# Kernel optimization log

Hardware: AMD Instinct MI355X
Metric: run time of the kernel (lower is better)

The kernel has to match this reference:

```python
import jax, jax.numpy as jnp
import numpy as np

BIG_NUMBER = 1e7   # repo constant used to mask padded adjacency slots
MAX_ITERS = 32     # params['flow_iters']


def _build_graph(B, N, D, valid_deg, seed=0):
    """Random d-regular-ish graph: each valid slot d holds a permutation of nodes,
    so every node has exactly `valid_deg` in-edges. in_indices[b,v,d] = (b,u,s)
    such that adj[b,u,s] == v. Padded slots (d >= valid_deg) hold the sentinel N
    and their in_indices point to a padded (near-zero-weight) flow entry."""
    rng = np.random.default_rng(seed)
    adj = np.full((B, N, D), N, dtype=np.int32)
    in_idx = np.zeros((B, N, D, 3), dtype=np.int32)
    in_idx[..., 0] = np.arange(B, dtype=np.int32)[:, None, None]
    in_idx[..., 2] = valid_deg  # padded slots -> flow[b, 0, valid_deg] (weight ~ 0)
    for b in range(B):
        for d in range(valid_deg):
            perm = rng.permutation(N).astype(np.int32)
            adj[b, :, d] = perm                      # edge u -> perm[u] via slot d
            inv = np.argsort(perm).astype(np.int32)  # inv[v] = u with perm[u] == v
            in_idx[b, :, d, 1] = inv
            in_idx[b, :, d, 2] = d
    return jnp.asarray(adj), jnp.asarray(in_idx)


def setup_inputs():
    B, N, D, VALID = 4, 100000, 16, 12
    key = jax.random.key(0)
    k1, k2 = jax.random.split(key)
    adj_lst, in_indices = _build_graph(B, N, D, VALID)
    return {
        "flow_proportions": jax.random.normal(k1, (B, N, D), dtype=jnp.float32),
        "demands": jax.random.normal(k2, (B, N, 1), dtype=jnp.float32),
        "adj_lst": adj_lst,
        "in_indices": in_indices,
        "num_nodes": N,
    }


def reference(flow_proportions, demands, adj_lst, in_indices, num_nodes):
    # --- masked softmax over neighbor slots (padded slots get -BIG_NUMBER) ---
    mask = (adj_lst == num_nodes).astype(flow_proportions.dtype)   # [B,N,D]
    masked = flow_proportions - BIG_NUMBER * mask
    weights = jax.nn.softmax(masked, axis=-1)                      # normalized_weights

    # --- mcf_solver: iterate flow <- weights * relu(inflow - demand) ---
    bidx = in_indices[..., 0]   # [B,N,D] batch index
    src = in_indices[..., 1]    # [B,N,D] source node of d-th in-edge
    slot = in_indices[..., 2]   # [B,N,D] slot of this node in source's adj list

    def step(flow, _):
        # gather incoming edge flows, sum -> inflow per node [B,N,1]
        inflow = flow[bidx, src, slot].sum(axis=-1, keepdims=True)
        new_flow = weights * jax.nn.relu(inflow - demands)
        return new_flow, None

    flow, _ = jax.lax.scan(step, jnp.zeros_like(weights), None, length=MAX_ITERS)
    # flow_cost (loss) = sum over nodes/slots of cost_fn(flow) = flow**2 here:
    # flow_cost = jnp.sum(flow * flow, axis=(1, 2))
    return flow
```

## Files before the change

kernel.cpp:

```cpp
#include <hip/hip_runtime.h>

#define DEG 16
#define E12 12
#define MAX_ITERS 32
#define BLK 1024
#define NCH 5
#define LDSH 20000
#define JMAX 96

typedef float f32x4 __attribute__((ext_vector_type(4)));

__device__ __forceinline__ float ld_sc0(const float* p) {
    return __hip_atomic_load((float*)p, __ATOMIC_RELAXED, __HIP_MEMORY_SCOPE_AGENT);
}
__device__ __forceinline__ unsigned ld_u32_sc0(const unsigned* p) {
    return __hip_atomic_load((unsigned*)p, __ATOMIC_RELAXED, __HIP_MEMORY_SCOPE_AGENT);
}
__device__ __forceinline__ void st_u32_sc0(unsigned* p, unsigned v) {
    __hip_atomic_store(p, v, __ATOMIC_RELAXED, __HIP_MEMORY_SCOPE_AGENT);
}

__device__ __forceinline__ f32x4 ld4_nw(const f32x4* p) {
    f32x4 v;
    asm volatile("global_load_dwordx4 %0, %1, off sc0" : "=v"(v) : "v"(p));
    return v;
}
__device__ __forceinline__ float ld1_l2(const float* p) {
    float v;
    asm volatile("global_load_dword %0, %1, off sc0\n\ts_waitcnt vmcnt(0)"
                 : "=v"(v) : "v"(p) : "memory");
    return v;
}
__device__ __forceinline__ void wait_vm0() {
    asm volatile("s_waitcnt vmcnt(0)" ::: "memory");
    __builtin_amdgcn_sched_barrier(0);
}

__device__ __forceinline__ int get_xcd() {
    unsigned x;
    asm volatile("s_getreg_b32 %0, hwreg(HW_REG_XCC_ID)" : "=s"(x));
    return (int)(x & 7u);
}

__device__ __forceinline__ void grid_barrier(unsigned* cnt, unsigned* gen,
                                             unsigned target, unsigned nblocks) {
    __syncthreads();
    if (threadIdx.x == 0) {
        __threadfence();
        unsigned arrived = __hip_atomic_fetch_add(cnt, 1u, __ATOMIC_ACQ_REL,
                                                  __HIP_MEMORY_SCOPE_AGENT);
        if (arrived == nblocks - 1u) {
            __hip_atomic_store(cnt, 0u, __ATOMIC_RELAXED, __HIP_MEMORY_SCOPE_AGENT);
            __hip_atomic_fetch_add(gen, 1u, __ATOMIC_RELEASE, __HIP_MEMORY_SCOPE_AGENT);
        } else {
            while (__hip_atomic_load(gen, __ATOMIC_RELAXED,
                                     __HIP_MEMORY_SCOPE_AGENT) < target)
                __builtin_amdgcn_s_sleep(2);
        }
        __threadfence();
    }
    __syncthreads();
}

__device__ __forceinline__ void xcd_barrier(unsigned* cnt, unsigned* gen,
                                            unsigned target, unsigned nblocks) {
    __syncthreads();
    if (threadIdx.x == 0) {
        unsigned arrived = __hip_atomic_fetch_add(cnt, 1u, __ATOMIC_RELEASE,
                                                  __HIP_MEMORY_SCOPE_WORKGROUP);
        if (arrived == nblocks - 1u) {
            __hip_atomic_store(cnt, 0u, __ATOMIC_RELAXED,
                               __HIP_MEMORY_SCOPE_WORKGROUP);
            __hip_atomic_fetch_add(gen, 1u, __ATOMIC_RELEASE,
                                   __HIP_MEMORY_SCOPE_WORKGROUP);
        } else {
            while (ld_u32_sc0(gen) < target)
                __builtin_amdgcn_s_sleep(2);
        }
    }
    __syncthreads();
}

__device__ __forceinline__ void softmax_row(const float* __restrict__ fp,
                                            const int* __restrict__ adj,
                                            float* __restrict__ wout,
                                            size_t base, int N) {
    const float4* f4 = (const float4*)(fp + base);
    const int4*   a4 = (const int4*)(adj + base);
    float v[DEG];
#pragma unroll
    for (int k = 0; k < DEG / 4; ++k) {
        float4 f = f4[k];
        int4   a = a4[k];
        v[4*k+0] = (a.x == N) ? f.x - 1e7f : f.x;
        v[4*k+1] = (a.y == N) ? f.y - 1e7f : f.y;
        v[4*k+2] = (a.z == N) ? f.z - 1e7f : f.z;
        v[4*k+3] = (a.w == N) ? f.w - 1e7f : f.w;
    }
    float m = v[0];
#pragma unroll
    for (int j = 1; j < DEG; ++j) m = fmaxf(m, v[j]);
    float s = 0.f;
#pragma unroll
    for (int j = 0; j < DEG; ++j) { v[j] = __expf(v[j] - m); s += v[j]; }
    float inv = 1.f / s;
    float4* w4 = (float4*)(wout + base);
#pragma unroll
    for (int k = 0; k < DEG / 4; ++k) {
        float4 o;
        o.x = v[4*k+0] * inv;
        o.y = v[4*k+1] * inv;
        o.z = v[4*k+2] * inv;
        o.w = v[4*k+3] * inv;
        w4[k] = o;
    }
}

__device__ __forceinline__ float node_acc12(const int* __restrict__ es,
                                            const float* __restrict__ ew,
                                            const float* __restrict__ Rc) {
    const int4*   s4 = (const int4*)es;
    const float4* w4 = (const float4*)ew;
    int4 a = s4[0], b = s4[1], c = s4[2];
    float4 x = w4[0], y = w4[1], z = w4[2];
    float acc;
    acc  = x.x * Rc[a.x];  acc += x.y * Rc[a.y];
    acc += x.z * Rc[a.z];  acc += x.w * Rc[a.w];
    acc += y.x * Rc[b.x];  acc += y.y * Rc[b.y];
    acc += y.z * Rc[b.z];  acc += y.w * Rc[b.w];
    acc += z.x * Rc[c.x];  acc += z.y * Rc[c.y];
    acc += z.z * Rc[c.z];  acc += z.w * Rc[c.w];
    return acc;
}

__device__ __forceinline__ void scale_row(float* __restrict__ wout, int g, float r) {
    float4* w4 = (float4*)(wout + (size_t)g * DEG);
#pragma unroll
    for (int k = 0; k < DEG / 4; ++k) {
        float4 v = w4[k];
        v.x *= r; v.y *= r; v.z *= r; v.w *= r;
        w4[k] = v;
    }
}

__device__ __forceinline__ void stage_issue(const float* src, int ce, int tid,
                                            f32x4* pv) {
    const int n4 = ce >> 2;
    const f32x4* s4 = (const f32x4*)src;
#pragma unroll
    for (int k = 0; k < 5; ++k) {
        int i4 = tid + k * BLK;
        if (i4 < n4) pv[k] = ld4_nw(s4 + i4);
    }
}
__device__ __forceinline__ void stage_write(float* L, const float* src, int ce,
                                            int tid, const f32x4* pv) {
    const int n4 = ce >> 2;
    f32x4* l4 = (f32x4*)L;
#pragma unroll
    for (int k = 0; k < 5; ++k) {
        int i4 = tid + k * BLK;
        if (i4 < n4) l4[i4] = pv[k];
    }
    for (int i = (n4 << 2) + tid; i < ce; i += BLK)
        L[i] = ld1_l2(src + i);
}

__global__ __launch_bounds__(BLK, 4)
void fused10_k(const float* __restrict__ fp, const int* __restrict__ adj,
               const int* __restrict__ in_idx, const float* __restrict__ dem,
               const int* __restrict__ nn, float* __restrict__ wout,
               char* __restrict__ wsb, int nodes) {
    __shared__ __align__(16) float lds2[2][LDSH];
    __shared__ int s_xcd, s_rank, s_mode, s_part, s_jbad;
    __shared__ int s_cm[NCH];
    __shared__ int s_off[NCH + 1];

    unsigned* g_cnt  = (unsigned*)(wsb);
    unsigned* g_gen  = (unsigned*)(wsb + 128);
    unsigned* blkcnt = (unsigned*)(wsb + 2304);
    unsigned* ovf    = (unsigned*)(wsb + 2432);
    unsigned* jovf   = (unsigned*)(wsb + 2436);
    int*   e_src   = (int*)(wsb + 4096);
    float* e_w     = (float*)(wsb + 4096 + (size_t)nodes * E12 * 4);
    float* Rf0     = (float*)((char*)e_w + (size_t)nodes * E12 * 4);
    float* Rf1     = Rf0 + nodes;
    float* slices  = Rf1 + nodes;
    uint2* regions = (uint2*)((char*)(slices) + (size_t)nodes * 16);

    const int N   = *nn;
    const int tid = (int)threadIdx.x;
    const int T   = (int)gridDim.x * BLK;
    const unsigned nblocks = gridDim.x;
    unsigned gb = 0;

    if (tid == 0) {
        int x = get_xcd();
        s_xcd  = x;
        s_rank = (int)__hip_atomic_fetch_add(&blkcnt[x], 1u, __ATOMIC_RELAXED,
                                             __HIP_MEMORY_SCOPE_AGENT);
    }
    __syncthreads();
    const int my_xcd  = s_xcd;
    const int my_rank = s_rank;

#pragma unroll
    for (int rep = 0; rep < 2; ++rep) {
        int g = (int)blockIdx.x * BLK + tid + rep * T;
        if (g < nodes) softmax_row(fp, adj, wout, (size_t)g * DEG, N);
    }
    grid_barrier(g_cnt, g_gen, ++gb, nblocks);

#pragma unroll
    for (int rep = 0; rep < 2; ++rep) {
        int g = (int)blockIdx.x * BLK + tid + rep * T;
        if (g >= nodes) continue;
        const int gbat = g / N;
        const int4* t4 = (const int4*)(in_idx + (size_t)g * 48);
        int cb[16], cs[16], cl[16];
#pragma unroll
        for (int q = 0; q < 4; ++q) {
            int4 qa = t4[3*q + 0];
            int4 qb = t4[3*q + 1];
            int4 qc = t4[3*q + 2];
            cb[4*q+0] = qa.x; cs[4*q+0] = qa.y; cl[4*q+0] = qa.z;
            cb[4*q+1] = qa.w; cs[4*q+1] = qb.x; cl[4*q+1] = qb.y;
            cb[4*q+2] = qb.z; cs[4*q+2] = qb.w; cl[4*q+2] = qc.x;
            cb[4*q+3] = qc.y; cs[4*q+3] = qc.z; cl[4*q+3] = qc.w;
        }
        float cw[16];
#pragma unroll
        for (int k = 0; k < 16; ++k)
            cw[k] = wout[((size_t)cb[k] * N + cs[k]) * DEG + cl[k]];
        bool bad = (cw[12] != 0.f) || (cw[13] != 0.f) ||
                   (cw[14] != 0.f) || (cw[15] != 0.f);
#pragma unroll
        for (int k = 0; k < E12; ++k)
            bad = bad || (cb[k] != gbat) || ((unsigned)cs[k] >= (unsigned)N);
        if (bad) st_u32_sc0(ovf, 1u);
        int4*   es4 = (int4*)(e_src + (size_t)g * E12);
        float4* ew4 = (float4*)(e_w + (size_t)g * E12);
        es4[0] = make_int4(cs[0], cs[1], cs[2], cs[3]);
        es4[1] = make_int4(cs[4], cs[5], cs[6], cs[7]);
        es4[2] = make_int4(cs[8], cs[9], cs[10], cs[11]);
        ew4[0] = make_float4(cw[0], cw[1], cw[2], cw[3]);
        ew4[1] = make_float4(cw[4], cw[5], cw[6], cw[7]);
        ew4[2] = make_float4(cw[8], cw[9], cw[10], cw[11]);
    }
    grid_barrier(g_cnt, g_gen, ++gb, nblocks);

    const int npb   = (N + 31) >> 5;
    const int chunk = (((N + NCH - 1) / NCH) + 3) & ~3;
    if (tid == 0) {
        unsigned cc[8];
#pragma unroll
        for (int x = 0; x < 8; ++x) cc[x] = ld_u32_sc0(&blkcnt[x]);
        bool ok = (4 * N == nodes) && (N > 0) && (N % 4 == 0) &&
                  (npb <= 4 * BLK) && (chunk <= LDSH) &&
                  (ld_u32_sc0(ovf) == 0u);
#pragma unroll
        for (int p = 0; p < 4; ++p)
            ok = ok && (cc[2*p] >= 32u || cc[2*p+1] >= 32u);
        s_mode = ok ? 1 : 0;
        s_part = (ok && cc[my_xcd] >= 32u && my_rank < 32) ? 1 : 0;
    }
    __syncthreads();
    const bool fast = (s_mode == 1);
    const bool part = (s_part == 1);

    if (fast) {
        const int batch = my_xcd >> 1;
        const int lbase = my_rank * npb;
        const int lim   = min(lbase + npb, N);
        float d[4];
        int   lno[4];
        bool  act[4];
        float r[4];
        unsigned long long mycnt = 0;
        uint2* reg = regions + (size_t)(my_xcd * 32 + my_rank) * (JMAX * BLK);

        if (part) {
            if (tid < NCH) s_cm[tid] = 0;
            __syncthreads();
            const int b1 = chunk, b2 = 2 * chunk, b3 = 3 * chunk, b4 = 4 * chunk;
            int c0 = 0, c1 = 0, c2 = 0, c3 = 0, c4 = 0;
#pragma unroll
            for (int s = 0; s < 4; ++s) {
                int l = lbase + s * BLK + tid;
                lno[s] = l;
                act[s] = (l < lim);
                d[s] = 0.f;
                if (act[s]) {
                    int g = batch * N + l;
                    d[s] = dem[g];
                    const int* es = e_src + (size_t)g * E12;
#pragma unroll
                    for (int k = 0; k < E12; ++k) {
                        int src = es[k];
                        int c = (src >= b1) + (src >= b2) + (src >= b3) +
                                (src >= b4);
                        c0 += (c == 0); c1 += (c == 1); c2 += (c == 2);
                        c3 += (c == 3); c4 += (c == 4);
                    }
                }
            }
            atomicMax(&s_cm[0], c0); atomicMax(&s_cm[1], c1);
            atomicMax(&s_cm[2], c2); atomicMax(&s_cm[3], c3);
            atomicMax(&s_cm[4], c4);
            __syncthreads();
            if (tid == 0) {
                s_off[0] = 0;
#pragma unroll
                for (int c = 0; c < NCH; ++c) s_off[c + 1] = s_off[c] + s_cm[c];
                if (s_off[NCH] > JMAX) st_u32_sc0(jovf, 1u);
            }
            __syncthreads();
            if (s_off[NCH] <= JMAX) {
                int cur0 = s_off[0], cur1 = s_off[1], cur2 = s_off[2],
                    cur3 = s_off[3], cur4 = s_off[4];
#pragma unroll
                for (int s = 0; s < 4; ++s) {
                    if (!act[s]) continue;
                    int g = batch * N + lno[s];
                    const int*   es = e_src + (size_t)g * E12;
                    const float* ew = e_w + (size_t)g * E12;
#pragma unroll
                    for (int k = 0; k < E12; ++k) {
                        int src = es[k];
                        float w = ew[k];
                        int c = (src >= b1) + (src >= b2) + (src >= b3) +
                                (src >= b4);
                        int j = (c == 0) ? cur0 : (c == 1) ? cur1
                               : (c == 2) ? cur2 : (c == 3) ? cur3 : cur4;
                        reg[(size_t)j * BLK + tid] =
                            make_uint2((unsigned)src | ((unsigned)s << 20),
                                       __float_as_uint(w));
                        cur0 += (c == 0); cur1 += (c == 1); cur2 += (c == 2);
                        cur3 += (c == 3); cur4 += (c == 4);
                    }
                }
                mycnt = (unsigned long long)(unsigned)(cur0 - s_off[0])
                      | ((unsigned long long)(unsigned)(cur1 - s_off[1]) << 8)
                      | ((unsigned long long)(unsigned)(cur2 - s_off[2]) << 16)
                      | ((unsigned long long)(unsigned)(cur3 - s_off[3]) << 24)
                      | ((unsigned long long)(unsigned)(cur4 - s_off[4]) << 32);
            }
        }
        grid_barrier(g_cnt, g_gen, ++gb, nblocks);
        if (tid == 0) s_jbad = (int)ld_u32_sc0(jovf);
        __syncthreads();

        if (s_jbad == 0) {
            if (!part) return;
            unsigned* xc = (unsigned*)(wsb + 256 + my_xcd * 256);
            unsigned* xg = (unsigned*)(wsb + 256 + my_xcd * 256 + 128);
            unsigned xb = 0;
            float* bufA = slices + (size_t)(2 * my_xcd + 0) * N;
            float* bufB = slices + (size_t)(2 * my_xcd + 1) * N;

#pragma unroll
            for (int s = 0; s < 4; ++s) {
                r[s] = fmaxf(-d[s], 0.f);
                if (act[s]) bufA[lno[s]] = r[s];
            }
            xcd_barrier(xc, xg, ++xb, 32u);

            const uint2* rp = reg + tid;
            float* Rin  = bufA;
            float* Rout = bufB;

#define PROC(PR)                                                       \
            {                                                          \
                float w_ = __uint_as_float((PR).y);                    \
                int idx_ = (int)((PR).x & 0xFFFFFu) - cbase;           \
                int tg_  = (int)((PR).x >> 20);                        \
                float wv_ = w_ * L[idx_];                              \
                a0 += (tg_ == 0) ? wv_ : 0.f;                          \
                a1 += (tg_ == 1) ? wv_ : 0.f;                          \
                a2 += (tg_ == 2) ? wv_ : 0.f;                          \
                a3 += (tg_ == 3) ? wv_ : 0.f;                          \
            }

            for (int t = 1; t < MAX_ITERS; ++t) {
                float a0 = 0.f, a1 = 0.f, a2 = 0.f, a3 = 0.f;
                f32x4 pv[5];
                {
                    const int ce0 = min(chunk, N);
                    stage_issue(Rin, ce0, tid, pv);
                    wait_vm0();
                    stage_write(lds2[0], Rin, ce0, tid, pv);
                }
                __syncthreads();
                for (int c = 0; c < NCH; ++c) {
                    const int cbase = c * chunk;
                    const float* L = lds2[c & 1];
                    const bool more = (c + 1 < NCH);
                    const float* src1 = Rin + (c + 1) * chunk;
                    const int ce1 = more ? min(chunk, N - (c + 1) * chunk) : 0;
                    if (more) stage_issue(src1, ce1, tid, pv);
                    const int jb = s_off[c];
                    const int je = jb + (int)((mycnt >> (8 * c)) & 255ull);
                    int j = jb;
                    for (; j + 4 <= je; j += 4) {
                        uint2 p0 = rp[(size_t)(j + 0) * BLK];
                        uint2 p1 = rp[(size_t)(j + 1) * BLK];
                        uint2 p2 = rp[(size_t)(j + 2) * BLK];
                        uint2 p3 = rp[(size_t)(j + 3) * BLK];
                        PROC(p0); PROC(p1); PROC(p2); PROC(p3);
                    }
                    for (; j < je; ++j) {
                        uint2 pr = rp[(size_t)j * BLK];
                        PROC(pr);
                    }
                    if (more) {
                        wait_vm0();
                        stage_write((float*)lds2[(c + 1) & 1], src1, ce1, tid, pv);
                    }
                    __syncthreads();
                }
                r[0] = fmaxf(a0 - d[0], 0.f);
                r[1] = fmaxf(a1 - d[1], 0.f);
                r[2] = fmaxf(a2 - d[2], 0.f);
                r[3] = fmaxf(a3 - d[3], 0.f);
                if (t < MAX_ITERS - 1) {
#pragma unroll
                    for (int s = 0; s < 4; ++s)
                        if (act[s]) Rout[lno[s]] = r[s];
                    xcd_barrier(xc, xg, ++xb, 32u);
                    float* tmp = Rin; Rin = Rout; Rout = tmp;
                }
            }
#undef PROC
#pragma unroll
            for (int s = 0; s < 4; ++s)
                if (act[s]) scale_row(wout, batch * N + lno[s], r[s]);
            return;
        }
    }

    {
        int g0 = (int)blockIdx.x * BLK + tid;
        int g1 = g0 + T;
        bool a0 = (g0 < nodes), a1 = (g1 < nodes);
        float d0 = a0 ? dem[g0] : 0.f;
        float d1 = a1 ? dem[g1] : 0.f;
        int base0 = a0 ? (g0 / N) * N : 0;
        int base1 = a1 ? (g1 / N) * N : 0;
        float r0 = fmaxf(-d0, 0.f), r1 = fmaxf(-d1, 0.f);
        if (a0) Rf0[g0] = r0;
        if (a1) Rf0[g1] = r1;
        grid_barrier(g_cnt, g_gen, ++gb, nblocks);
        const float* Rc = Rf0;
        float*       Rn = Rf1;
        for (int t = 1; t < MAX_ITERS; ++t) {
            if (a0) r0 = fmaxf(node_acc12(e_src + (size_t)g0 * E12,
                                          e_w + (size_t)g0 * E12,
                                          Rc + base0) - d0, 0.f);
            if (a1) r1 = fmaxf(node_acc12(e_src + (size_t)g1 * E12,
                                          e_w + (size_t)g1 * E12,
                                          Rc + base1) - d1, 0.f);
            if (t < MAX_ITERS - 1) {
                if (a0) Rn[g0] = r0;
                if (a1) Rn[g1] = r1;
                grid_barrier(g_cnt, g_gen, ++gb, nblocks);
                float* tmp = (float*)Rc; Rc = Rn; Rn = tmp;
            }
        }
        if (a0) scale_row(wout, g0, r0);
        if (a1) scale_row(wout, g1, r1);
    }
}

__global__ void softmax_k(const float* __restrict__ fp, const int* __restrict__ adj,
                          const int* __restrict__ nn, float* __restrict__ wout,
                          int nodes) {
    int i = blockIdx.x * blockDim.x + threadIdx.x;
    if (i >= nodes) return;
    softmax_row(fp, adj, wout, (size_t)i * DEG, *nn);
}

__global__ void gather_k(const int* __restrict__ in_idx, const float* __restrict__ w,
                         const int* __restrict__ nn, int* __restrict__ e_srcO,
                         float* __restrict__ e_wO, int edges) {
    int e = blockIdx.x * blockDim.x + threadIdx.x;
    if (e >= edges) return;
    const int N = *nn;
    size_t e3 = 3 * (size_t)e;
    int fi = in_idx[e3] * N + in_idx[e3 + 1];
    e_srcO[e] = fi;
    e_wO[e]   = w[(size_t)fi * DEG + in_idx[e3 + 2]];
}

__global__ void iter_k(const int* __restrict__ e_srcO, const float* __restrict__ e_wO,
                       const float* __restrict__ dem, const float* __restrict__ Rin,
                       float* __restrict__ Rout, int nodes) {
    int i = blockIdx.x * blockDim.x + threadIdx.x;
    if (i >= nodes) return;
    const size_t base = (size_t)i * DEG;
    const int4*   s4 = (const int4*)(e_srcO + base);
    const float4* w4 = (const float4*)(e_wO + base);
    float acc = 0.f;
#pragma unroll
    for (int k = 0; k < DEG / 4; ++k) {
        int4   s = s4[k];
        float4 w = w4[k];
        acc += w.x * Rin[s.x];
        acc += w.y * Rin[s.y];
        acc += w.z * Rin[s.z];
        acc += w.w * Rin[s.w];
    }
    float r = acc - dem[i];
    Rout[i] = r > 0.f ? r : 0.f;
}

__global__ void final_k(const float* __restrict__ w, const float* __restrict__ R,
                        float* __restrict__ out, int nodes) {
    int i = blockIdx.x * blockDim.x + threadIdx.x;
    if (i >= nodes) return;
    scale_row((float*)w, i, R[i]);
    (void)out;
}

extern "C" void kernel_launch(void* const* d_in, const int* in_sizes, int n_in,
                              void* d_out, int out_size, void* d_ws, size_t ws_size,
                              hipStream_t stream) {
    const float* fp  = (const float*)d_in[0];
    const float* dem = (const float*)d_in[1];
    const int*   adj = (const int*)d_in[2];
    const int*   idx = (const int*)d_in[3];
    const int*   nn  = (const int*)d_in[4];

    const int edges = in_sizes[0];
    const int nodes = in_sizes[1];

    float* weights = (float*)d_out;
    char*  ws      = (char*)d_ws;

    int dev = 0, cus = 0, maxBlk = 0;
    hipGetDevice(&dev);
    hipDeviceGetAttribute(&cus, hipDeviceAttributeMultiprocessorCount, dev);
    hipOccupancyMaxActiveBlocksPerMultiprocessor(&maxBlk, (const void*)fused10_k,
                                                 BLK, 0);

    const size_t need = 4096 + (size_t)nodes * (E12 * 8 + 8 + 16)
                      + (size_t)256 * JMAX * BLK * 8;
    const int grid = cus;

    const bool fused_ok = (maxBlk >= 1) && (cus >= 16) &&
                          ((long long)grid * BLK * 2 >= nodes) &&
                          (ws_size >= need) && (nodes % 4 == 0);

    if (fused_ok) {
        hipMemsetAsync(ws, 0, 4096, stream);
        void* args[] = { (void*)&fp, (void*)&adj, (void*)&idx, (void*)&dem,
                         (void*)&nn, (void*)&weights, (void*)&ws, (void*)&nodes };
        hipLaunchCooperativeKernel((const void*)fused10_k, dim3(grid), dim3(BLK),
                                   args, 0, stream);
    } else {
        int*   e_srcO = (int*)ws;
        float* e_wO   = (float*)(ws + (size_t)edges * sizeof(int));
        float* R0     = (float*)(ws + (size_t)edges * 8);
        float* R1     = R0 + nodes;
        const int blk = 256;
        const int gn = (nodes + blk - 1) / blk;
        const int ge = (edges + blk - 1) / blk;
        hipMemsetAsync(R0, 0, (size_t)nodes * sizeof(float), stream);
        softmax_k<<<gn, blk, 0, stream>>>(fp, adj, nn, weights, nodes);
        gather_k<<<ge, blk, 0, stream>>>(idx, weights, nn, e_srcO, e_wO, edges);
        float* a = R0;
        float* b = R1;
        for (int t = 0; t < MAX_ITERS; ++t) {
            iter_k<<<gn, blk, 0, stream>>>(e_srcO, e_wO, dem, a, b, nodes);
            float* tmp = a; a = b; b = tmp;
        }
        final_k<<<gn, blk, 0, stream>>>(weights, a, (float*)d_out, nodes);
    }
}
```

Baseline: 1.025 ms.

## Keep per-chunk edge lists in registers and accumulate via LDS atomics

Edges for each block are now bucketed into 8 source chunks, with fixed slot capacity per chunk, using block-wide atomicAdd offsets instead of per-thread max-count padding. Each thread loads its fixed set of 40 edge records into registers once, then accumulates each iteration's contributions into a shared-memory accumulator with LDS atomics. The LDS staging chunk is smaller. This removes per-iteration global reads of edge metadata and the padded per-thread edge loops, at the cost of LDS atomic contention, more registers, and more staging phases and barriers per iteration.

```diff
diff --git a/kernel.cpp b/kernel.cpp
--- a/kernel.cpp
+++ b/kernel.cpp
@@ -4,15 +4,15 @@
 #define E12 12
 #define MAX_ITERS 32
 #define BLK 1024
-#define NCH 5
-#define LDSH 20000
+#define NCH 8
+#define KSLOT 5
+#define SLOTS (NCH * KSLOT)
+#define LDSH 12544
+#define UST 4
 #define JMAX 96
 
 typedef float f32x4 __attribute__((ext_vector_type(4)));
 
-__device__ __forceinline__ float ld_sc0(const float* p) {
-    return __hip_atomic_load((float*)p, __ATOMIC_RELAXED, __HIP_MEMORY_SCOPE_AGENT);
-}
 __device__ __forceinline__ unsigned ld_u32_sc0(const unsigned* p) {
     return __hip_atomic_load((unsigned*)p, __ATOMIC_RELAXED, __HIP_MEMORY_SCOPE_AGENT);
 }
@@ -148,7 +148,7 @@
     const int n4 = ce >> 2;
     const f32x4* s4 = (const f32x4*)src;
 #pragma unroll
-    for (int k = 0; k < 5; ++k) {
+    for (int k = 0; k < UST; ++k) {
         int i4 = tid + k * BLK;
         if (i4 < n4) pv[k] = ld4_nw(s4 + i4);
     }
@@ -158,7 +158,7 @@
     const int n4 = ce >> 2;
     f32x4* l4 = (f32x4*)L;
 #pragma unroll
-    for (int k = 0; k < 5; ++k) {
+    for (int k = 0; k < UST; ++k) {
         int i4 = tid + k * BLK;
         if (i4 < n4) l4[i4] = pv[k];
     }
@@ -167,14 +167,14 @@
 }
 
 __global__ __launch_bounds__(BLK, 4)
-void fused10_k(const float* __restrict__ fp, const int* __restrict__ adj,
+void fused12_k(const float* __restrict__ fp, const int* __restrict__ adj,
                const int* __restrict__ in_idx, const float* __restrict__ dem,
                const int* __restrict__ nn, float* __restrict__ wout,
                char* __restrict__ wsb, int nodes) {
     __shared__ __align__(16) float lds2[2][LDSH];
+    __shared__ float accS[4 * BLK];
+    __shared__ int s_bc[NCH];
     __shared__ int s_xcd, s_rank, s_mode, s_part, s_jbad;
-    __shared__ int s_cm[NCH];
-    __shared__ int s_off[NCH + 1];
 
     unsigned* g_cnt  = (unsigned*)(wsb);
     unsigned* g_gen  = (unsigned*)(wsb + 128);
@@ -273,77 +273,74 @@
         const int lbase = my_rank * npb;
         const int lim   = min(lbase + npb, N);
         float d[4];
-        int   lno[4];
-        bool  act[4];
         float r[4];
-        unsigned long long mycnt = 0;
-        uint2* reg = regions + (size_t)(my_xcd * 32 + my_rank) * (JMAX * BLK);
+        uint2* reg = regions + (size_t)(my_xcd * 32 + my_rank) * (SLOTS * BLK);
 
         if (part) {
-            if (tid < NCH) s_cm[tid] = 0;
+            if (tid < NCH) s_bc[tid] = 0;
             __syncthreads();
-            const int b1 = chunk, b2 = 2 * chunk, b3 = 3 * chunk, b4 = 4 * chunk;
-            int c0 = 0, c1 = 0, c2 = 0, c3 = 0, c4 = 0;
+            const int b1 = chunk, b2 = 2*chunk, b3 = 3*chunk, b4 = 4*chunk,
+                      b5 = 5*chunk, b6 = 6*chunk, b7 = 7*chunk;
+            int c0=0,c1=0,c2=0,c3=0,c4=0,c5=0,c6=0,c7=0;
 #pragma unroll
             for (int s = 0; s < 4; ++s) {
                 int l = lbase + s * BLK + tid;
-                lno[s] = l;
-                act[s] = (l < lim);
                 d[s] = 0.f;
-                if (act[s]) {
+                if (l < lim) {
                     int g = batch * N + l;
                     d[s] = dem[g];
                     const int* es = e_src + (size_t)g * E12;
 #pragma unroll
                     for (int k = 0; k < E12; ++k) {
                         int src = es[k];
-                        int c = (src >= b1) + (src >= b2) + (src >= b3) +
-                                (src >= b4);
-                        c0 += (c == 0); c1 += (c == 1); c2 += (c == 2);
-                        c3 += (c == 3); c4 += (c == 4);
+                        int c = (src>=b1)+(src>=b2)+(src>=b3)+(src>=b4)+
+                                (src>=b5)+(src>=b6)+(src>=b7);
+                        c0 += (c==0); c1 += (c==1); c2 += (c==2); c3 += (c==3);
+                        c4 += (c==4); c5 += (c==5); c6 += (c==6); c7 += (c==7);
                     }
                 }
             }
-            atomicMax(&s_cm[0], c0); atomicMax(&s_cm[1], c1);
-            atomicMax(&s_cm[2], c2); atomicMax(&s_cm[3], c3);
-            atomicMax(&s_cm[4], c4);
+            int u0 = atomicAdd(&s_bc[0], c0);
+            int u1 = atomicAdd(&s_bc[1], c1);
+            int u2 = atomicAdd(&s_bc[2], c2);
+            int u3 = atomicAdd(&s_bc[3], c3);
+            int u4 = atomicAdd(&s_bc[4], c4);
+            int u5 = atomicAdd(&s_bc[5], c5);
+            int u6 = atomicAdd(&s_bc[6], c6);
+            int u7 = atomicAdd(&s_bc[7], c7);
+#pragma unroll
+            for (int s = 0; s < 4; ++s) {
+                int l = lbase + s * BLK + tid;
+                if (l >= lim) continue;
+                int g = batch * N + l;
+                const int*   es = e_src + (size_t)g * E12;
+                const float* ew = e_w + (size_t)g * E12;
+                const unsigned tgt = (unsigned)(s * BLK + tid) << 14;
+#pragma unroll
+                for (int k = 0; k < E12; ++k) {
+                    int src = es[k];
+                    float w = ew[k];
+                    int c = (src>=b1)+(src>=b2)+(src>=b3)+(src>=b4)+
+                            (src>=b5)+(src>=b6)+(src>=b7);
+                    int p = (c==0)?u0:(c==1)?u1:(c==2)?u2:(c==3)?u3:
+                            (c==4)?u4:(c==5)?u5:(c==6)?u6:u7;
+                    if (p < KSLOT * BLK) {
+                        int kk = p >> 10;
+                        int ow = p & (BLK - 1);
+                        reg[((size_t)(c * KSLOT + kk)) * BLK + ow] =
+                            make_uint2((unsigned)(src - c * chunk) | tgt,
+                                       __float_as_uint(w));
+                    }
+                    u0 += (c==0); u1 += (c==1); u2 += (c==2); u3 += (c==3);
+                    u4 += (c==4); u5 += (c==5); u6 += (c==6); u7 += (c==7);
+                }
+            }
             __syncthreads();
             if (tid == 0) {
-                s_off[0] = 0;
-#pragma unroll
-                for (int c = 0; c < NCH; ++c) s_off[c + 1] = s_off[c] + s_cm[c];
-                if (s_off[NCH] > JMAX) st_u32_sc0(jovf, 1u);
-            }
-            __syncthreads();
-            if (s_off[NCH] <= JMAX) {
-                int cur0 = s_off[0], cur1 = s_off[1], cur2 = s_off[2],
-                    cur3 = s_off[3], cur4 = s_off[4];
-#pragma unroll
-                for (int s = 0; s < 4; ++s) {
-                    if (!act[s]) continue;
-                    int g = batch * N + lno[s];
-                    const int*   es = e_src + (size_t)g * E12;
-                    const float* ew = e_w + (size_t)g * E12;
-#pragma unroll
-                    for (int k = 0; k < E12; ++k) {
-                        int src = es[k];
-                        float w = ew[k];
-                        int c = (src >= b1) + (src >= b2) + (src >= b3) +
-                                (src >= b4);
-                        int j = (c == 0) ? cur0 : (c == 1) ? cur1
-                               : (c == 2) ? cur2 : (c == 3) ? cur3 : cur4;
-                        reg[(size_t)j * BLK + tid] =
-                            make_uint2((unsigned)src | ((unsigned)s << 20),
-                                       __float_as_uint(w));
-                        cur0 += (c == 0); cur1 += (c == 1); cur2 += (c == 2);
-                        cur3 += (c == 3); cur4 += (c == 4);
-                    }
-                }
-                mycnt = (unsigned long long)(unsigned)(cur0 - s_off[0])
-                      | ((unsigned long long)(unsigned)(cur1 - s_off[1]) << 8)
-                      | ((unsigned long long)(unsigned)(cur2 - s_off[2]) << 16)
-                      | ((unsigned long long)(unsigned)(cur3 - s_off[3]) << 24)
-                      | ((unsigned long long)(unsigned)(cur4 - s_off[4]) << 32);
+                bool bad = false;
+#pragma unroll
+                for (int c = 0; c < NCH; ++c) bad = bad || (s_bc[c] > KSLOT*BLK);
+                if (bad) st_u32_sc0(jovf, 1u);
             }
         }
         grid_barrier(g_cnt, g_gen, ++gb, nblocks);
@@ -352,6 +349,22 @@
 
         if (s_jbad == 0) {
             if (!part) return;
+            unsigned mmeta[SLOTS];
+            float    mw[SLOTS];
+#pragma unroll
+            for (int c = 0; c < NCH; ++c) {
+#pragma unroll
+                for (int k = 0; k < KSLOT; ++k) {
+                    uint2 e = make_uint2(0u, 0u);
+                    if (k * BLK + tid < s_bc[c])
+                        e = reg[((size_t)(c * KSLOT + k)) * BLK + tid];
+                    mmeta[c * KSLOT + k] = e.x;
+                    mw[c * KSLOT + k]    = __uint_as_float(e.y);
+                }
+            }
+#pragma unroll
+            for (int s = 0; s < 4; ++s) accS[s * BLK + tid] = 0.f;
+
             unsigned* xc = (unsigned*)(wsb + 256 + my_xcd * 256);
             unsigned* xg = (unsigned*)(wsb + 256 + my_xcd * 256 + 128);
             unsigned xb = 0;
@@ -360,30 +373,17 @@
 
 #pragma unroll
             for (int s = 0; s < 4; ++s) {
+                int l = lbase + s * BLK + tid;
                 r[s] = fmaxf(-d[s], 0.f);
-                if (act[s]) bufA[lno[s]] = r[s];
+                if (l < lim) bufA[l] = r[s];
             }
             xcd_barrier(xc, xg, ++xb, 32u);
 
-            const uint2* rp = reg + tid;
             float* Rin  = bufA;
             float* Rout = bufB;
 
-#define PROC(PR)                                                       \
-            {                                                          \
-                float w_ = __uint_as_float((PR).y);                    \
-                int idx_ = (int)((PR).x & 0xFFFFFu) - cbase;           \
-                int tg_  = (int)((PR).x >> 20);                        \
-                float wv_ = w_ * L[idx_];                              \
-                a0 += (tg_ == 0) ? wv_ : 0.f;                          \
-                a1 += (tg_ == 1) ? wv_ : 0.f;                          \
-                a2 += (tg_ == 2) ? wv_ : 0.f;                          \
-                a3 += (tg_ == 3) ? wv_ : 0.f;                          \
-            }
-
             for (int t = 1; t < MAX_ITERS; ++t) {
-                float a0 = 0.f, a1 = 0.f, a2 = 0.f, a3 = 0.f;
-                f32x4 pv[5];
+                f32x4 pv[UST];
                 {
                     const int ce0 = min(chunk, N);
                     stage_issue(Rin, ce0, tid, pv);
@@ -391,49 +391,54 @@
                     stage_write(lds2[0], Rin, ce0, tid, pv);
                 }
                 __syncthreads();
+#pragma unroll
                 for (int c = 0; c < NCH; ++c) {
-                    const int cbase = c * chunk;
                     const float* L = lds2[c & 1];
-                    const bool more = (c + 1 < NCH);
-                    const float* src1 = Rin + (c + 1) * chunk;
-                    const int ce1 = more ? min(chunk, N - (c + 1) * chunk) : 0;
-                    if (more) stage_issue(src1, ce1, tid, pv);
-                    const int jb = s_off[c];
-                    const int je = jb + (int)((mycnt >> (8 * c)) & 255ull);
-                    int j = jb;
-                    for (; j + 4 <= je; j += 4) {
-                        uint2 p0 = rp[(size_t)(j + 0) * BLK];
-                        uint2 p1 = rp[(size_t)(j + 1) * BLK];
-                        uint2 p2 = rp[(size_t)(j + 2) * BLK];
-                        uint2 p3 = rp[(size_t)(j + 3) * BLK];
-                        PROC(p0); PROC(p1); PROC(p2); PROC(p3);
-                    }
-                    for (; j < je; ++j) {
-                        uint2 pr = rp[(size_t)j * BLK];
-                        PROC(pr);
-                    }
-                    if (more) {
+                    if (c + 1 < NCH) {
+                        const float* src1 = Rin + (c + 1) * chunk;
+                        const int ce1 = min(chunk, N - (c + 1) * chunk);
+                        stage_issue(src1, ce1, tid, pv);
+#pragma unroll
+                        for (int k = 0; k < KSLOT; ++k) {
+                            unsigned m = mmeta[c * KSLOT + k];
+                            float    w = mw[c * KSLOT + k];
+                            float   Rv = L[m & 16383u];
+                            atomicAdd(&accS[m >> 14], w * Rv);
+                        }
                         wait_vm0();
                         stage_write((float*)lds2[(c + 1) & 1], src1, ce1, tid, pv);
+                    } else {
+#pragma unroll
+                        for (int k = 0; k < KSLOT; ++k) {
+                            unsigned m = mmeta[c * KSLOT + k];
+                            float    w = mw[c * KSLOT + k];
+                            float   Rv = L[m & 16383u];
+                            atomicAdd(&accS[m >> 14], w * Rv);
+                        }
                     }
                     __syncthreads();
                 }
-                r[0] = fmaxf(a0 - d[0], 0.f);
-                r[1] = fmaxf(a1 - d[1], 0.f);
-                r[2] = fmaxf(a2 - d[2], 0.f);
-                r[3] = fmaxf(a3 - d[3], 0.f);
+#pragma unroll
+                for (int s = 0; s < 4; ++s) {
+                    float a = accS[s * BLK + tid];
+                    accS[s * BLK + tid] = 0.f;
+                    r[s] = fmaxf(a - d[s], 0.f);
+                }
                 if (t < MAX_ITERS - 1) {
 #pragma unroll
-                    for (int s = 0; s < 4; ++s)
-                        if (act[s]) Rout[lno[s]] = r[s];
+                    for (int s = 0; s < 4; ++s) {
+                        int l = lbase + s * BLK + tid;
+                        if (l < lim) Rout[l] = r[s];
+                    }
                     xcd_barrier(xc, xg, ++xb, 32u);
                     float* tmp = Rin; Rin = Rout; Rout = tmp;
                 }
             }
-#undef PROC
-#pragma unroll
-            for (int s = 0; s < 4; ++s)
-                if (act[s]) scale_row(wout, batch * N + lno[s], r[s]);
+#pragma unroll
+            for (int s = 0; s < 4; ++s) {
+                int l = lbase + s * BLK + tid;
+                if (l < lim) scale_row(wout, batch * N + l, r[s]);
+            }
             return;
         }
     }
@@ -539,7 +544,7 @@
     int dev = 0, cus = 0, maxBlk = 0;
     hipGetDevice(&dev);
     hipDeviceGetAttribute(&cus, hipDeviceAttributeMultiprocessorCount, dev);
-    hipOccupancyMaxActiveBlocksPerMultiprocessor(&maxBlk, (const void*)fused10_k,
+    hipOccupancyMaxActiveBlocksPerMultiprocessor(&maxBlk, (const void*)fused12_k,
                                                  BLK, 0);
 
     const size_t need = 4096 + (size_t)nodes * (E12 * 8 + 8 + 16)
@@ -554,7 +559,7 @@
         hipMemsetAsync(ws, 0, 4096, stream);
         void* args[] = { (void*)&fp, (void*)&adj, (void*)&idx, (void*)&dem,
                          (void*)&nn, (void*)&weights, (void*)&ws, (void*)&nodes };
-        hipLaunchCooperativeKernel((const void*)fused10_k, dim3(grid), dim3(BLK),
+        hipLaunchCooperativeKernel((const void*)fused12_k, dim3(grid), dim3(BLK),
                                    args, 0, stream);
     } else {
         int*   e_srcO = (int*)ws;
```

Result: no change. 1.027 ms (+0.2%).

## Replace per-XCD barrier with per-block progress flags gating each staged chunk

Applied to the files above, without the earlier changes.

The all-blocks XCD barrier after each flow iteration is replaced by a per-block progress counter. Each block publishes its finished iteration number, and before staging a chunk of the residual vector into LDS a block waits only on the flags of the blocks that produce that chunk. This lets blocks move ahead without waiting for every peer, and overlaps waiting with the processing of earlier chunks. In exchange, visibility now rests on a relaxed flag store after __syncthreads with no explicit fence, and there is extra polling per chunk.

```diff
diff --git a/kernel.cpp b/kernel.cpp
--- a/kernel.cpp
+++ b/kernel.cpp
@@ -10,9 +10,6 @@
 
 typedef float f32x4 __attribute__((ext_vector_type(4)));
 
-__device__ __forceinline__ float ld_sc0(const float* p) {
-    return __hip_atomic_load((float*)p, __ATOMIC_RELAXED, __HIP_MEMORY_SCOPE_AGENT);
-}
 __device__ __forceinline__ unsigned ld_u32_sc0(const unsigned* p) {
     return __hip_atomic_load((unsigned*)p, __ATOMIC_RELAXED, __HIP_MEMORY_SCOPE_AGENT);
 }
@@ -62,21 +59,11 @@
     __syncthreads();
 }
 
-__device__ __forceinline__ void xcd_barrier(unsigned* cnt, unsigned* gen,
-                                            unsigned target, unsigned nblocks) {
-    __syncthreads();
-    if (threadIdx.x == 0) {
-        unsigned arrived = __hip_atomic_fetch_add(cnt, 1u, __ATOMIC_RELEASE,
-                                                  __HIP_MEMORY_SCOPE_WORKGROUP);
-        if (arrived == nblocks - 1u) {
-            __hip_atomic_store(cnt, 0u, __ATOMIC_RELAXED,
-                               __HIP_MEMORY_SCOPE_WORKGROUP);
-            __hip_atomic_fetch_add(gen, 1u, __ATOMIC_RELEASE,
-                                   __HIP_MEMORY_SCOPE_WORKGROUP);
-        } else {
-            while (ld_u32_sc0(gen) < target)
-                __builtin_amdgcn_s_sleep(2);
-        }
+__device__ __forceinline__ void gate_chunk(unsigned* flg, int rlo, int rhi,
+                                           unsigned need, int tid) {
+    if (tid <= (rhi - rlo)) {
+        while (ld_u32_sc0(&flg[rlo + tid]) < need)
+            __builtin_amdgcn_s_sleep(1);
     }
     __syncthreads();
 }
@@ -167,7 +154,7 @@
 }
 
 __global__ __launch_bounds__(BLK, 4)
-void fused10_k(const float* __restrict__ fp, const int* __restrict__ adj,
+void fused13_k(const float* __restrict__ fp, const int* __restrict__ adj,
                const int* __restrict__ in_idx, const float* __restrict__ dem,
                const int* __restrict__ nn, float* __restrict__ wout,
                char* __restrict__ wsb, int nodes) {
@@ -352,9 +339,7 @@
 
         if (s_jbad == 0) {
             if (!part) return;
-            unsigned* xc = (unsigned*)(wsb + 256 + my_xcd * 256);
-            unsigned* xg = (unsigned*)(wsb + 256 + my_xcd * 256 + 128);
-            unsigned xb = 0;
+            unsigned* flg = (unsigned*)(wsb + 256 + my_xcd * 256);
             float* bufA = slices + (size_t)(2 * my_xcd + 0) * N;
             float* bufB = slices + (size_t)(2 * my_xcd + 1) * N;
 
@@ -363,7 +348,8 @@
                 r[s] = fmaxf(-d[s], 0.f);
                 if (act[s]) bufA[lno[s]] = r[s];
             }
-            xcd_barrier(xc, xg, ++xb, 32u);
+            __syncthreads();
+            if (tid == 0) st_u32_sc0(&flg[my_rank], 1u);
 
             const uint2* rp = reg + tid;
             float* Rin  = bufA;
@@ -382,10 +368,12 @@
             }
 
             for (int t = 1; t < MAX_ITERS; ++t) {
+                const unsigned need = (unsigned)t;
                 float a0 = 0.f, a1 = 0.f, a2 = 0.f, a3 = 0.f;
                 f32x4 pv[5];
                 {
                     const int ce0 = min(chunk, N);
+                    gate_chunk(flg, 0, min(31, (ce0 - 1) / npb), need, tid);
                     stage_issue(Rin, ce0, tid, pv);
                     wait_vm0();
                     stage_write(lds2[0], Rin, ce0, tid, pv);
@@ -395,9 +383,14 @@
                     const int cbase = c * chunk;
                     const float* L = lds2[c & 1];
                     const bool more = (c + 1 < NCH);
-                    const float* src1 = Rin + (c + 1) * chunk;
-                    const int ce1 = more ? min(chunk, N - (c + 1) * chunk) : 0;
-                    if (more) stage_issue(src1, ce1, tid, pv);
+                    const int sb1 = (c + 1) * chunk;
+                    const float* src1 = Rin + sb1;
+                    const int ce1 = more ? min(chunk, N - sb1) : 0;
+                    if (more && ce1 > 0) {
+                        gate_chunk(flg, sb1 / npb,
+                                   min(31, (sb1 + ce1 - 1) / npb), need, tid);
+                        stage_issue(src1, ce1, tid, pv);
+                    }
                     const int jb = s_off[c];
                     const int je = jb + (int)((mycnt >> (8 * c)) & 255ull);
                     int j = jb;
@@ -412,7 +405,7 @@
                         uint2 pr = rp[(size_t)j * BLK];
                         PROC(pr);
                     }
-                    if (more) {
+                    if (more && ce1 > 0) {
                         wait_vm0();
                         stage_write((float*)lds2[(c + 1) & 1], src1, ce1, tid, pv);
                     }
@@ -426,7 +419,8 @@
 #pragma unroll
                     for (int s = 0; s < 4; ++s)
                         if (act[s]) Rout[lno[s]] = r[s];
-                    xcd_barrier(xc, xg, ++xb, 32u);
+                    __syncthreads();
+                    if (tid == 0) st_u32_sc0(&flg[my_rank], (unsigned)(t + 1));
                     float* tmp = Rin; Rin = Rout; Rout = tmp;
                 }
             }
@@ -539,7 +533,7 @@
     int dev = 0, cus = 0, maxBlk = 0;
     hipGetDevice(&dev);
     hipDeviceGetAttribute(&cus, hipDeviceAttributeMultiprocessorCount, dev);
-    hipOccupancyMaxActiveBlocksPerMultiprocessor(&maxBlk, (const void*)fused10_k,
+    hipOccupancyMaxActiveBlocksPerMultiprocessor(&maxBlk, (const void*)fused13_k,
                                                  BLK, 0);
 
     const size_t need = 4096 + (size_t)nodes * (E12 * 8 + 8 + 16)
@@ -554,7 +548,7 @@
         hipMemsetAsync(ws, 0, 4096, stream);
         void* args[] = { (void*)&fp, (void*)&adj, (void*)&idx, (void*)&dem,
                          (void*)&nn, (void*)&weights, (void*)&ws, (void*)&nodes };
-        hipLaunchCooperativeKernel((const void*)fused10_k, dim3(grid), dim3(BLK),
+        hipLaunchCooperativeKernel((const void*)fused13_k, dim3(grid), dim3(BLK),
                                    args, 0, stream);
     } else {
         int*   e_srcO = (int*)ws;
```

After: 1.028 ms. No clear change (+0.3%).
